# Optimization experiments

Measured on AMD Instinct MI355X. Metric: run time of the kernel, lower is better.

The kernel has to match this reference:

```python
import jax, jax.numpy as jnp
import numpy as np

D_MODEL = 1024
NUM_HEADS = 16
HEAD_DIM = D_MODEL // NUM_HEADS
FF_DIM = 4096
EPS = 1e-5


def _layer_norm(x, gamma, beta):
    mu = jnp.mean(x, axis=-1, keepdims=True)
    var = jnp.var(x, axis=-1, keepdims=True)
    return (x - mu) * jax.lax.rsqrt(var + EPS) * gamma + beta


def setup_inputs() -> dict:
    key0 = jax.random.key(0)
    ks = jax.random.split(key0, 20)
    s = 0.02
    B, S = 2, 2048
    inp = {
        'value': jax.random.normal(ks[0], (B, S, D_MODEL), jnp.float32),
        'key': jax.random.normal(ks[1], (B, S, D_MODEL), jnp.float32),
        'query': jax.random.normal(ks[2], (B, S, D_MODEL), jnp.float32),
        # attention projections (stored [in, out]; y = x @ W + b)
        'wq': jax.random.normal(ks[3], (D_MODEL, D_MODEL), jnp.float32) * s,
        'bq': jnp.zeros((D_MODEL,), jnp.float32),
        'wk': jax.random.normal(ks[4], (D_MODEL, D_MODEL), jnp.float32) * s,
        'bk': jnp.zeros((D_MODEL,), jnp.float32),
        'wv': jax.random.normal(ks[5], (D_MODEL, D_MODEL), jnp.float32) * s,
        'bv': jnp.zeros((D_MODEL,), jnp.float32),
        'wo': jax.random.normal(ks[6], (D_MODEL, D_MODEL), jnp.float32) * s,
        'bo': jnp.zeros((D_MODEL,), jnp.float32),
        # layernorm 1
        'g1': jnp.ones((D_MODEL,), jnp.float32),
        'beta1': jnp.zeros((D_MODEL,), jnp.float32),
        # feed-forward
        'w1': jax.random.normal(ks[7], (D_MODEL, FF_DIM), jnp.float32) * s,
        'b1': jnp.zeros((FF_DIM,), jnp.float32),
        'w2': jax.random.normal(ks[8], (FF_DIM, D_MODEL), jnp.float32) * s,
        'b2': jnp.zeros((D_MODEL,), jnp.float32),
        # layernorm 2
        'g2': jnp.ones((D_MODEL,), jnp.float32),
        'beta2': jnp.zeros((D_MODEL,), jnp.float32),
    }
    return inp


def reference(value, key, query, wq, bq, wk, bk, wv, bv, wo, bo,
              g1, beta1, w1, b1, w2, b2, g2, beta2):
    B, S, _ = query.shape
    # QKV projections -> [B, S, H, Dh]
    Q = (query @ wq + bq).reshape(B, S, NUM_HEADS, HEAD_DIM)
    K = (key @ wk + bk).reshape(B, S, NUM_HEADS, HEAD_DIM)
    V = (value @ wv + bv).reshape(B, S, NUM_HEADS, HEAD_DIM)
    # scaled dot-product attention (full score matrix, as in source)
    energy = jnp.einsum('bqhd,bkhd->bhqk', Q, K) / jnp.sqrt(jnp.float32(HEAD_DIM))
    attn = jax.nn.softmax(energy, axis=-1)
    out = jnp.einsum('bhqk,bkhd->bqhd', attn, V).reshape(B, S, D_MODEL)
    attn_out = out @ wo + bo
    # residual + norm1 (dropout is identity in eval)
    x = _layer_norm(attn_out + query, g1, beta1)
    # feed-forward
    ff = jax.nn.relu(x @ w1 + b1) @ w2 + b2
    # residual + norm2
    return _layer_norm(ff + x, g2, beta2)
```

## Files before the change

### kernel.cpp

```cpp
#include <hip/hip_runtime.h>
#include <hip/hip_bf16.h>
#include <cstdint>
#include <math.h>

typedef __bf16 bf16_t;
typedef __attribute__((ext_vector_type(2))) __bf16 bf16x2;
typedef __attribute__((ext_vector_type(4))) __bf16 bf16x4;
typedef __attribute__((ext_vector_type(8))) __bf16 bf16x8;
typedef __attribute__((ext_vector_type(4))) float f32x4;
typedef __attribute__((ext_vector_type(16))) float f32x16;
typedef __attribute__((ext_vector_type(2))) int int2v;
typedef __attribute__((ext_vector_type(4))) int int4v;

#define B_SZ 2
#define S_SZ 2048
#define D_MODEL 1024
#define NUM_HEADS 16
#define HEAD_DIM 64
#define FF_DIM 4096
#define M_ROWS (B_SZ * S_SZ)

#define CF 0.180336880f
#define THRC 2.0f

__device__ __forceinline__ float fexp2(float x) { return __builtin_amdgcn_exp2f(x); }

__device__ __forceinline__ void gload_lds16(const void* g, void* lds) {
    __builtin_amdgcn_global_load_lds(
        (const __attribute__((address_space(1))) void*)(uintptr_t)g,
        (__attribute__((address_space(3))) void*)(uint32_t)(uintptr_t)lds,
        16, 0, 0);
}

__device__ __forceinline__ f32x4 mfma16(bf16x8 a, bf16x8 b, f32x4 c) {
    return __builtin_amdgcn_mfma_f32_16x16x32_bf16(a, b, c, 0, 0, 0);
}
__device__ __forceinline__ f32x16 mfma32(bf16x8 a, bf16x8 b, f32x16 c) {
    return __builtin_amdgcn_mfma_f32_32x32x16_bf16(a, b, c, 0, 0, 0);
}
__device__ __forceinline__ int2v plswap(int a, int b) {
    return __builtin_amdgcn_permlane32_swap(a, b, false, false);
}
__device__ __forceinline__ int packbf(float a, float b) {
    bf16x2 t; t[0] = (bf16_t)a; t[1] = (bf16_t)b;
    return __builtin_bit_cast(int, t);
}

__device__ __forceinline__ int xcd_swz(int lin, int nwg) {
    return (lin & 7) * (nwg >> 3) + (lin >> 3);
}

__global__ __launch_bounds__(256) void cast3_f32_bf16(const float* __restrict__ in0,
                                                      const float* __restrict__ in1,
                                                      const float* __restrict__ in2,
                                                      bf16_t* __restrict__ out0,
                                                      bf16_t* __restrict__ out1,
                                                      bf16_t* __restrict__ out2) {
    int which = blockIdx.x >> 12;
    int blk = blockIdx.x & 4095;
    const float* in = which == 0 ? in0 : which == 1 ? in1 : in2;
    bf16_t* out = which == 0 ? out0 : which == 1 ? out1 : out2;
    size_t i = ((size_t)blk * 256 + threadIdx.x) * 4;
    float4 v = *(const float4*)(in + i);
    bf16x4 o;
    o[0] = (bf16_t)v.x; o[1] = (bf16_t)v.y; o[2] = (bf16_t)v.z; o[3] = (bf16_t)v.w;
    *(bf16x4*)(out + i) = o;
}

__global__ __launch_bounds__(256) void transpose_cast_w4(const float* __restrict__ W0,
                                                         const float* __restrict__ W1,
                                                         const float* __restrict__ W2,
                                                         const float* __restrict__ W3,
                                                         bf16_t* __restrict__ T0,
                                                         bf16_t* __restrict__ T1,
                                                         bf16_t* __restrict__ T2,
                                                         bf16_t* __restrict__ T3) {
    __shared__ float t[32][33];
    const int K = 1024, N = 1024;
    const float* W = blockIdx.z == 0 ? W0 : blockIdx.z == 1 ? W1 : blockIdx.z == 2 ? W2 : W3;
    bf16_t* WT = blockIdx.z == 0 ? T0 : blockIdx.z == 1 ? T1 : blockIdx.z == 2 ? T2 : T3;
    int tid = threadIdx.x;
    int rr = tid >> 3, cc = (tid & 7) * 4;
    int k0 = blockIdx.x * 32, n0 = blockIdx.y * 32;
    float4 v = *(const float4*)(W + (size_t)(k0 + rr) * N + n0 + cc);
    t[rr][cc + 0] = v.x; t[rr][cc + 1] = v.y; t[rr][cc + 2] = v.z; t[rr][cc + 3] = v.w;
    __syncthreads();
    bf16x4 o;
    o[0] = (bf16_t)t[cc + 0][rr]; o[1] = (bf16_t)t[cc + 1][rr];
    o[2] = (bf16_t)t[cc + 2][rr]; o[3] = (bf16_t)t[cc + 3][rr];
    *(bf16x4*)(WT + (size_t)(n0 + rr) * K + k0 + cc) = o;
}

__global__ __launch_bounds__(256) void transpose_cast_w(const float* __restrict__ W,
                                                        bf16_t* __restrict__ WT,
                                                        int K, int N) {
    __shared__ float t[32][33];
    int tid = threadIdx.x;
    int rr = tid >> 3, cc = (tid & 7) * 4;
    int k0 = blockIdx.x * 32, n0 = blockIdx.y * 32;
    float4 v = *(const float4*)(W + (size_t)(k0 + rr) * N + n0 + cc);
    t[rr][cc + 0] = v.x; t[rr][cc + 1] = v.y; t[rr][cc + 2] = v.z; t[rr][cc + 3] = v.w;
    __syncthreads();
    bf16x4 o;
    o[0] = (bf16_t)t[cc + 0][rr]; o[1] = (bf16_t)t[cc + 1][rr];
    o[2] = (bf16_t)t[cc + 2][rr]; o[3] = (bf16_t)t[cc + 3][rr];
    *(bf16x4*)(WT + (size_t)(n0 + rr) * K + k0 + cc) = o;
}

__global__ __launch_bounds__(256) void transpose_v(const bf16_t* __restrict__ Vp,
                                                   bf16_t* __restrict__ VT) {
    __shared__ bf16_t t[32][34];
    int tid = threadIdx.x;
    int rr = tid >> 3, cc = (tid & 7) * 4;
    int bh = blockIdx.z;
    int b = bh >> 4, h = bh & 15;
    int s0 = blockIdx.x * 32, d0 = blockIdx.y * 32;
    bf16x4 v = *(const bf16x4*)(Vp + ((size_t)(b * S_SZ + s0 + rr)) * D_MODEL + h * HEAD_DIM + d0 + cc);
    t[rr][cc + 0] = v[0]; t[rr][cc + 1] = v[1]; t[rr][cc + 2] = v[2]; t[rr][cc + 3] = v[3];
    __syncthreads();
    bf16x4 o;
    o[0] = t[cc + 0][rr]; o[1] = t[cc + 1][rr]; o[2] = t[cc + 2][rr]; o[3] = t[cc + 3][rr];
    *(bf16x4*)(VT + ((size_t)(bh * HEAD_DIM + d0 + rr)) * S_SZ + s0 + cc) = o;
}

template<int NJT, bool RELU, bool OUT_BF16, bool OUT_F32>
__device__ __forceinline__ void gemm8p_core(const bf16_t* __restrict__ Ag, int lda,
                                            const bf16_t* __restrict__ Bg, int ldb,
                                            const float* __restrict__ bias, bool useBias,
                                            float* __restrict__ Cf,
                                            bf16_t* __restrict__ Cb,
                                            int N, int Klen, int m0, int n0,
                                            bf16_t* sA, bf16_t* sB) {
    constexpr int BELE = 8192 * NJT;
    constexpr int NBQ = 2 * NJT;
    const int tid = threadIdx.x;
    const int lane = tid & 63, w = tid >> 6;
    const int l31 = lane & 31, hi = lane >> 5;
    const int wm = (w >> 2) * 128;
    const int wn = (w & 3) * (32 * NJT);
    const int rs7 = l31 & 7;

    const int scol = ((tid & 7) ^ ((tid >> 3) & 7)) * 8;
    const bf16_t* aSrc = Ag + (size_t)(m0 + (tid >> 3)) * lda + scol;
    const bf16_t* bSrc = Bg + (size_t)(n0 + (tid >> 3)) * ldb + scol;

    f32x16 acc[4][NJT];
#pragma unroll
    for (int it = 0; it < 4; it++)
#pragma unroll
        for (int jt = 0; jt < NJT; jt++)
#pragma unroll
            for (int e = 0; e < 16; e++) acc[it][jt][e] = 0.f;

    auto stA = [&](int buf, int q, int k0) {
        gload_lds16(aSrc + (size_t)(q * 64) * lda + k0, sA + buf * 16384 + q * 4096 + tid * 8);
    };
    auto stB = [&](int buf, int q, int k0) {
        gload_lds16(bSrc + (size_t)(q * 64) * ldb + k0, sB + buf * BELE + q * 4096 + tid * 8);
    };

    bf16x8 a[4], b[NJT];
    auto RD = [&](int buf, int ks) {
        const bf16_t* bA = sA + buf * 16384;
        const bf16_t* bB = sB + buf * BELE;
        const int cs = ((((ks << 1) | hi)) ^ rs7) << 3;
#pragma unroll
        for (int it = 0; it < 4; it++)
            a[it] = *(const bf16x8*)(bA + (wm + it * 32 + l31) * 64 + cs);
#pragma unroll
        for (int jt = 0; jt < NJT; jt++)
            b[jt] = *(const bf16x8*)(bB + (wn + jt * 32 + l31) * 64 + cs);
    };
    auto MM = [&]() {
        __builtin_amdgcn_s_setprio(1);
#pragma unroll
        for (int it = 0; it < 4; it++)
#pragma unroll
            for (int jt = 0; jt < NJT; jt++)
                acc[it][jt] = mfma32(a[it], b[jt], acc[it][jt]);
        __builtin_amdgcn_s_setprio(0);
    };

#define LGKM0() do { asm volatile("s_waitcnt lgkmcnt(0)" ::: "memory"); \
                     __builtin_amdgcn_sched_barrier(0); } while (0)

    const int nk = Klen >> 6;
#pragma unroll
    for (int q = 0; q < 4; q++) stA(0, q, 0);
#pragma unroll
    for (int q = 0; q < NBQ; q++) stB(0, q, 0);
    asm volatile("s_waitcnt vmcnt(0)" ::: "memory");
    __builtin_amdgcn_s_barrier();

    for (int t = 0; t < nk; ++t) {
        const int buf = t & 1, nb = buf ^ 1;
        const int kn = (t + 1) << 6;
        const bool hn = (t + 1 < nk);
        RD(buf, 0);
        if (hn) { stA(nb, 0, kn); stA(nb, 1, kn); stA(nb, 2, kn); }
        LGKM0();
        MM();
        RD(buf, 1);
        if (hn) { stA(nb, 3, kn); stB(nb, 0, kn); if (NBQ > 1) stB(nb, 1, kn); }
        LGKM0();
        MM();
        RD(buf, 2);
        if (hn && NBQ > 2) { stB(nb, 2, kn); stB(nb, 3, kn); }
        LGKM0();
        MM();
        RD(buf, 3);
        LGKM0();
        MM();
        asm volatile("s_waitcnt vmcnt(0)" ::: "memory");
        __builtin_amdgcn_s_barrier();
    }
#undef LGKM0

#pragma unroll
    for (int it = 0; it < 4; it++) {
#pragma unroll
        for (int jt = 0; jt < NJT; jt++) {
            const int n = n0 + wn + jt * 32 + l31;
            const float bv = useBias ? bias[n] : 0.f;
#pragma unroll
            for (int e = 0; e < 16; e++) {
                const int mrow = m0 + wm + it * 32 + (e & 3) + ((e >> 2) << 3) + hi * 4;
                float val = acc[it][jt][e] + bv;
                if (RELU) val = fmaxf(val, 0.f);
                if (OUT_F32) Cf[(size_t)mrow * N + n] = val;
                if (OUT_BF16) Cb[(size_t)mrow * N + n] = (bf16_t)val;
            }
        }
    }
}

template<int NJT, bool RELU>
__global__ __launch_bounds__(512, 1) void gemm8p(const bf16_t* __restrict__ A, int lda,
                                                 const bf16_t* __restrict__ Bt, int ldb,
                                                 const float* __restrict__ bias,
                                                 bf16_t* __restrict__ Cb0,
                                                 bf16_t* __restrict__ Cb1,
                                                 int N, int Klen) {
    __shared__ bf16_t sA[2 * 16384];
    __shared__ bf16_t sB[2 * 8192 * NJT];
    const int lin = blockIdx.x + gridDim.x * (blockIdx.y + gridDim.y * blockIdx.z);
    const int nwg = gridDim.x * gridDim.y * gridDim.z;
    const int sz = xcd_swz(lin, nwg);
    const int bx = sz % gridDim.x;
    const int rest = sz / gridDim.x;
    const int by = rest % gridDim.y;
    const int bz = rest / gridDim.y;
    const int koff = bz * Klen;
    gemm8p_core<NJT, RELU, true, false>(A + koff, lda, Bt + koff, ldb,
                                        bias, bz == 0,
                                        nullptr, bz ? Cb1 : Cb0, N, Klen,
                                        bx * 256, by * (128 * NJT), sA, sB);
}

template<int NJT, bool RELU>
__global__ __launch_bounds__(512, 1) void gemm8p_b(const bf16_t* __restrict__ A, int lda,
                                                   const bf16_t* __restrict__ Bt, int ldb,
                                                   const float* __restrict__ bias,
                                                   bf16_t* __restrict__ Cb,
                                                   int N, int Klen) {
    __shared__ bf16_t sA[2 * 16384];
    __shared__ bf16_t sB[2 * 8192 * NJT];
    const int lin = blockIdx.x + gridDim.x * (blockIdx.y + gridDim.y * blockIdx.z);
    const int nwg = gridDim.x * gridDim.y * gridDim.z;
    const int sz = xcd_swz(lin, nwg);
    const int bx = sz % gridDim.x;
    const int rest = sz / gridDim.x;
    const int by = rest % gridDim.y;
    gemm8p_core<NJT, RELU, true, false>(A, lda, Bt, ldb, bias, true,
                                        nullptr, Cb, N, Klen,
                                        bx * 256, by * (128 * NJT), sA, sB);
}

__global__ __launch_bounds__(512, 1) void gemm_qkv8p(const bf16_t* __restrict__ A0,
                                                     const bf16_t* __restrict__ A1,
                                                     const bf16_t* __restrict__ A2,
                                                     const bf16_t* __restrict__ B0,
                                                     const bf16_t* __restrict__ B1,
                                                     const bf16_t* __restrict__ B2,
                                                     const float* __restrict__ b0,
                                                     const float* __restrict__ b1,
                                                     const float* __restrict__ b2,
                                                     bf16_t* __restrict__ C0,
                                                     bf16_t* __restrict__ C1,
                                                     bf16_t* __restrict__ C2) {
    __shared__ bf16_t sA[2 * 16384];
    __shared__ bf16_t sB[2 * 16384];
    const int lin = blockIdx.x + gridDim.x * (blockIdx.y + gridDim.y * blockIdx.z);
    const int nwg = gridDim.x * gridDim.y * gridDim.z;
    const int sz = xcd_swz(lin, nwg);
    const int bx = sz % gridDim.x;
    const int rest = sz / gridDim.x;
    const int by = rest % gridDim.y;
    const int bz = rest / gridDim.y;
    const bf16_t* A = bz == 0 ? A0 : bz == 1 ? A1 : A2;
    const bf16_t* Bt = bz == 0 ? B0 : bz == 1 ? B1 : B2;
    const float* bias = bz == 0 ? b0 : bz == 1 ? b1 : b2;
    bf16_t* C = bz == 0 ? C0 : bz == 1 ? C1 : C2;
    gemm8p_core<2, false, true, false>(A, 1024, Bt, 1024, bias, true,
                                       nullptr, C, 1024, 1024, bx * 256, by * 256, sA, sB);
}

__device__ __forceinline__ void flash_tile(
    const char* kt, const char* vt, int l31, int hi,
    const bf16x8 (&bq)[4],
    f32x16& o0, f32x16& o1, float& mC, float& l_run)
{
    bf16x8 ak[4];
#pragma unroll
    for (int kb = 0; kb < 4; kb++)
        ak[kb] = *(const bf16x8*)(kt + l31 * 128 + (((kb << 1) | hi) ^ (l31 & 7)) * 16);
    bf16x8 av[4];
#pragma unroll
    for (int db = 0; db < 2; db++)
#pragma unroll
        for (int kb = 0; kb < 2; kb++)
            av[db * 2 + kb] = *(const bf16x8*)(vt + (db * 32 + l31) * 64 + ((((kb << 1) | hi)) ^ ((l31 >> 1) & 3)) * 16);

    f32x16 s;
#pragma unroll
    for (int e = 0; e < 16; e++) s[e] = 0.f;
#pragma unroll
    for (int kb = 0; kb < 4; kb++) s = mfma32(ak[kb], bq[kb], s);

    float ma = fmaxf(fmaxf(s[0], s[1]), fmaxf(s[2], s[3]));
    float mb = fmaxf(fmaxf(s[4], s[5]), fmaxf(s[6], s[7]));
    float mc = fmaxf(fmaxf(s[8], s[9]), fmaxf(s[10], s[11]));
    float md = fmaxf(fmaxf(s[12], s[13]), fmaxf(s[14], s[15]));
    float pmaxC = fmaxf(fmaxf(ma, mb), fmaxf(mc, md)) * CF;

    if (!__all(pmaxC <= mC + THRC)) {
        int2v pr = plswap(__float_as_int(pmaxC), __float_as_int(pmaxC));
        float rowmaxC = fmaxf(__int_as_float(pr[0]), __int_as_float(pr[1]));
        float mnewC = fmaxf(mC, rowmaxC);
        float alpha = fexp2(mC - mnewC);
        mC = mnewC;
        l_run *= alpha;
#pragma unroll
        for (int e = 0; e < 16; e++) { o0[e] *= alpha; o1[e] *= alpha; }
    }

#pragma unroll
    for (int e = 0; e < 16; e++) s[e] = fexp2(__builtin_fmaf(s[e], CF, -mC));
    float t0 = (s[0] + s[1]) + (s[2] + s[3]);
    float t1 = (s[4] + s[5]) + (s[6] + s[7]);
    float t2 = (s[8] + s[9]) + (s[10] + s[11]);
    float t3 = (s[12] + s[13]) + (s[14] + s[15]);
    l_run += (t0 + t1) + (t2 + t3);

#pragma unroll
    for (int kb2 = 0; kb2 < 2; kb2++) {
        const int bse = kb2 * 8;
        int W0 = packbf(s[bse + 0], s[bse + 1]);
        int W1 = packbf(s[bse + 2], s[bse + 3]);
        int W2 = packbf(s[bse + 4], s[bse + 5]);
        int W3 = packbf(s[bse + 6], s[bse + 7]);
        int2v r02 = plswap(W0, W2);
        int2v r13 = plswap(W1, W3);
        int4v fw; fw[0] = r02[0]; fw[1] = r13[0]; fw[2] = r02[1]; fw[3] = r13[1];
        bf16x8 pf = __builtin_bit_cast(bf16x8, fw);
        o0 = mfma32(av[kb2], pf, o0);
        o1 = mfma32(av[2 + kb2], pf, o1);
    }
}

__global__ __launch_bounds__(256) void flash_attn(const bf16_t* __restrict__ Qp,
                                                  const bf16_t* __restrict__ Kp,
                                                  const bf16_t* __restrict__ VT,
                                                  bf16_t* __restrict__ Oa) {
    __shared__ alignas(16) char lds[2][2][8192];
    const int tid = threadIdx.x;
    const int lane = tid & 63;
    const int wave = tid >> 6;
    const int half = wave >> 1;
    const int qt = wave & 1;
    const int l31 = lane & 31, hi = lane >> 5;

    const int lin = blockIdx.x + (blockIdx.y << 5) + (blockIdx.z << 9);
    const int swz = (lin & 7) * 128 + (lin >> 3);
    const int qb = swz & 31;
    const int h = (swz >> 5) & 15;
    const int b = swz >> 9;

    const int q0 = qb * 64 + qt * 32;

    const bf16_t* Qb = Qp + (size_t)b * S_SZ * D_MODEL + h * HEAD_DIM;
    const bf16_t* Kb = Kp + (size_t)b * S_SZ * D_MODEL + h * HEAD_DIM;
    const bf16_t* Vb = VT + ((size_t)(b * NUM_HEADS + h) * HEAD_DIM) * S_SZ;

    const int sh = wave & 1;
    const int skvbase = sh * (S_SZ / 2);
    const bool kRole = wave < 2;

    const bf16_t* src_run;
    size_t inner_stride;
    size_t tile_stride;
    char* dst0;
    char* dst1;
    if (kRole) {
        src_run = Kb + (size_t)(skvbase + (lane >> 3)) * D_MODEL + ((lane & 7) ^ (lane >> 3)) * 8;
        inner_stride = (size_t)8 * D_MODEL;
        tile_stride = (size_t)32 * D_MODEL;
        dst0 = &lds[0][sh][0] + lane * 16;
        dst1 = &lds[1][sh][0] + lane * 16;
    } else {
        src_run = Vb + (size_t)(lane >> 2) * S_SZ + skvbase + ((lane & 3) ^ ((lane >> 3) & 3)) * 8;
        inner_stride = (size_t)16 * S_SZ;
        tile_stride = 32;
        dst0 = &lds[0][sh][4096] + lane * 16;
        dst1 = &lds[1][sh][4096] + lane * 16;
    }

    bf16x8 bq[4];
#pragma unroll
    for (int kb = 0; kb < 4; kb++)
        bq[kb] = *(const bf16x8*)(Qb + (size_t)(q0 + l31) * D_MODEL + kb * 16 + hi * 8);

    f32x16 o0, o1;
#pragma unroll
    for (int e = 0; e < 16; e++) { o0[e] = 0.f; o1[e] = 0.f; }
    float mC = -1e30f, l_run = 0.f;

    const char* kt0 = &lds[0][half][0];
    const char* vt0 = &lds[0][half][4096];
    const char* kt1 = &lds[1][half][0];
    const char* vt1 = &lds[1][half][4096];

#pragma unroll
    for (int ii = 0; ii < 4; ii++)
        gload_lds16(src_run + ii * inner_stride, dst0 + ii * 1024);
    src_run += tile_stride;
    __syncthreads();

    for (int t = 0; t < 32; t += 2) {
#pragma unroll
        for (int ii = 0; ii < 4; ii++)
            gload_lds16(src_run + ii * inner_stride, dst1 + ii * 1024);
        src_run += tile_stride;
        flash_tile(kt0, vt0, l31, hi, bq, o0, o1, mC, l_run);
        __syncthreads();

        if (t + 2 < 32) {
#pragma unroll
            for (int ii = 0; ii < 4; ii++)
                gload_lds16(src_run + ii * inner_stride, dst0 + ii * 1024);
            src_run += tile_stride;
        }
        flash_tile(kt1, vt1, l31, hi, bq, o0, o1, mC, l_run);
        __syncthreads();
    }

    int2v lp = plswap(__float_as_int(l_run), __float_as_int(l_run));
    l_run = __int_as_float(lp[0]) + __int_as_float(lp[1]);

    float (*obuf)[2][64] = (float (*)[2][64])(&lds[0][0][0]);
    float (*mrg)[64][2] = (float (*)[64][2])(&lds[0][0][0] + 16384);
    if (half == 1) {
        mrg[qt][lane][0] = mC;
        mrg[qt][lane][1] = l_run;
#pragma unroll
        for (int e = 0; e < 16; e++) {
            obuf[e][qt][lane] = o0[e];
            obuf[16 + e][qt][lane] = o1[e];
        }
    }
    __syncthreads();
    if (half == 0) {
        const float m2C = mrg[qt][lane][0], l2 = mrg[qt][lane][1];
        const float mm = fmaxf(mC, m2C);
        const float e1 = fexp2(mC - mm);
        const float e2 = fexp2(m2C - mm);
        const float linv = 1.f / (l_run * e1 + l2 * e2);
        bf16_t* Orow = Oa + ((size_t)b * S_SZ + q0 + l31) * D_MODEL + h * HEAD_DIM;
#pragma unroll
        for (int db = 0; db < 2; db++) {
#pragma unroll
            for (int rq = 0; rq < 4; rq++) {
                bf16x4 st;
#pragma unroll
                for (int i = 0; i < 4; i++) {
                    const int e = rq * 4 + i;
                    const float own = db ? o1[e] : o0[e];
                    const float oth = obuf[db * 16 + e][qt][lane];
                    st[i] = (bf16_t)((own * e1 + oth * e2) * linv);
                }
                *(bf16x4*)(Orow + db * 32 + rq * 8 + hi * 4) = st;
            }
        }
    }
}

__global__ __launch_bounds__(256) void ln_fused(const bf16_t* __restrict__ A,
                                                const bf16_t* __restrict__ A2,
                                                const float* __restrict__ R,
                                                const float* __restrict__ gamma,
                                                const float* __restrict__ beta,
                                                float* __restrict__ Xf,
                                                bf16_t* __restrict__ Xb) {
    __shared__ float red[8];
    int row = blockIdx.x, tid = threadIdx.x;
    size_t base = (size_t)row * D_MODEL + tid * 4;
    bf16x4 a = *(const bf16x4*)(A + base);
    bf16x4 a2 = *(const bf16x4*)(A2 + base);
    float4 rv = *(const float4*)(R + base);
    float v0 = (float)a[0] + (float)a2[0] + rv.x;
    float v1 = (float)a[1] + (float)a2[1] + rv.y;
    float v2 = (float)a[2] + (float)a2[2] + rv.z;
    float v3 = (float)a[3] + (float)a2[3] + rv.w;
    float s = v0 + v1 + v2 + v3;
    float q = v0 * v0 + v1 * v1 + v2 * v2 + v3 * v3;
#pragma unroll
    for (int off = 32; off; off >>= 1) { s += __shfl_down(s, off); q += __shfl_down(q, off); }
    if ((tid & 63) == 0) { red[tid >> 6] = s; red[4 + (tid >> 6)] = q; }
    __syncthreads();
    s = red[0] + red[1] + red[2] + red[3];
    q = red[4] + red[5] + red[6] + red[7];
    float mean = s * (1.f / D_MODEL);
    float var = q * (1.f / D_MODEL) - mean * mean;
    float rstd = rsqrtf(var + 1e-5f);
    float4 gm = *(const float4*)(gamma + tid * 4);
    float4 bt = *(const float4*)(beta + tid * 4);
    float y0 = (v0 - mean) * rstd * gm.x + bt.x;
    float y1 = (v1 - mean) * rstd * gm.y + bt.y;
    float y2 = (v2 - mean) * rstd * gm.z + bt.z;
    float y3 = (v3 - mean) * rstd * gm.w + bt.w;
    float4 yo; yo.x = y0; yo.y = y1; yo.z = y2; yo.w = y3;
    *(float4*)(Xf + base) = yo;
    if (Xb) {
        bf16x4 ob; ob[0] = (bf16_t)y0; ob[1] = (bf16_t)y1; ob[2] = (bf16_t)y2; ob[3] = (bf16_t)y3;
        *(bf16x4*)(Xb + base) = ob;
    }
}

extern "C" void kernel_launch(void* const* d_in, const int* in_sizes, int n_in,
                              void* d_out, int out_size, void* d_ws, size_t ws_size,
                              hipStream_t stream) {
    const float* value = (const float*)d_in[0];
    const float* key   = (const float*)d_in[1];
    const float* query = (const float*)d_in[2];
    const float* wq = (const float*)d_in[3];
    const float* bq = (const float*)d_in[4];
    const float* wk = (const float*)d_in[5];
    const float* bk = (const float*)d_in[6];
    const float* wv = (const float*)d_in[7];
    const float* bv = (const float*)d_in[8];
    const float* wo = (const float*)d_in[9];
    const float* bo = (const float*)d_in[10];
    const float* g1 = (const float*)d_in[11];
    const float* beta1 = (const float*)d_in[12];
    const float* w1 = (const float*)d_in[13];
    const float* b1 = (const float*)d_in[14];
    const float* w2 = (const float*)d_in[15];
    const float* b2 = (const float*)d_in[16];
    const float* g2 = (const float*)d_in[17];
    const float* beta2 = (const float*)d_in[18];
    (void)in_sizes; (void)n_in; (void)out_size; (void)ws_size;

    const size_t MB = 1ull << 20;
    char* ws = (char*)d_ws;
    bf16_t* wqT = (bf16_t*)(ws + 0 * MB);
    bf16_t* wkT = (bf16_t*)(ws + 2 * MB);
    bf16_t* wvT = (bf16_t*)(ws + 4 * MB);
    bf16_t* woT = (bf16_t*)(ws + 6 * MB);
    bf16_t* w1T = (bf16_t*)(ws + 8 * MB);
    bf16_t* w2T = (bf16_t*)(ws + 16 * MB);
    bf16_t* q_bf = (bf16_t*)(ws + 24 * MB);
    bf16_t* k_bf = (bf16_t*)(ws + 32 * MB);
    bf16_t* v_bf = (bf16_t*)(ws + 40 * MB);
    bf16_t* Qp  = (bf16_t*)(ws + 48 * MB);
    bf16_t* Kp  = (bf16_t*)(ws + 56 * MB);
    bf16_t* Vp  = (bf16_t*)(ws + 64 * MB);
    bf16_t* VT  = (bf16_t*)(ws + 72 * MB);
    bf16_t* attn = (bf16_t*)(ws + 24 * MB);
    bf16_t* woP0 = (bf16_t*)(ws + 32 * MB);
    bf16_t* woP1 = (bf16_t*)(ws + 42 * MB);
    float*  x_f = (float*)(ws + 80 * MB);
    bf16_t* x_b = (bf16_t*)(ws + 24 * MB);
    bf16_t* h_b = (bf16_t*)(ws + 32 * MB);
    bf16_t* ffP0 = (bf16_t*)(ws + 64 * MB);
    bf16_t* ffP1 = (bf16_t*)(ws + 72 * MB);

    dim3 blk(256);
    dim3 blk512(512);

    cast3_f32_bf16<<<12288, blk, 0, stream>>>(query, key, value, q_bf, k_bf, v_bf);
    transpose_cast_w4<<<dim3(32, 32, 4), blk, 0, stream>>>(wq, wk, wv, wo, wqT, wkT, wvT, woT);
    transpose_cast_w<<<dim3(32, 128), blk, 0, stream>>>(w1, w1T, 1024, 4096);
    transpose_cast_w<<<dim3(128, 32), blk, 0, stream>>>(w2, w2T, 4096, 1024);

    gemm_qkv8p<<<dim3(16, 4, 3), blk512, 0, stream>>>(q_bf, k_bf, v_bf, wqT, wkT, wvT,
                                                      bq, bk, bv, Qp, Kp, Vp);

    transpose_v<<<dim3(64, 2, 32), blk, 0, stream>>>(Vp, VT);

    flash_attn<<<dim3(32, 16, 2), blk, 0, stream>>>(Qp, Kp, VT, attn);

    gemm8p<1, false><<<dim3(16, 8, 2), blk512, 0, stream>>>(attn, 1024, woT, 1024, bo, woP0, woP1, D_MODEL, 512);

    ln_fused<<<4096, blk, 0, stream>>>(woP0, woP1, query, g1, beta1, x_f, x_b);

    gemm8p_b<2, true><<<dim3(16, 16, 1), blk512, 0, stream>>>(x_b, 1024, w1T, 1024, b1, h_b, FF_DIM, 1024);

    gemm8p<1, false><<<dim3(16, 8, 2), blk512, 0, stream>>>(h_b, 4096, w2T, 4096, b2, ffP0, ffP1, D_MODEL, 2048);

    ln_fused<<<4096, blk, 0, stream>>>(ffP0, ffP1, x_f, g2, beta2, (float*)d_out, nullptr);
}
```

Before: 231.9 us.

## Merge input prep kernels and fuse V transpose into QKV GEMM epilogue

Merges the activation cast and all weight transpose-casts into one prep kernel, replacing four launches with one. The V projection GEMM epilogue now writes V already transposed per head into the VT layout, which removes the separate transpose_v kernel and its round trip of V through memory. The tradeoff is that the epilogue's transposed stores are 8-byte scattered writes with a stride of S, so they coalesce less well than the row-major path.

```diff
diff --git a/kernel.cpp b/kernel.cpp
--- a/kernel.cpp
+++ b/kernel.cpp
@@ -50,77 +50,53 @@
     return (lin & 7) * (nwg >> 3) + (lin >> 3);
 }
 
-__global__ __launch_bounds__(256) void cast3_f32_bf16(const float* __restrict__ in0,
-                                                      const float* __restrict__ in1,
-                                                      const float* __restrict__ in2,
-                                                      bf16_t* __restrict__ out0,
-                                                      bf16_t* __restrict__ out1,
-                                                      bf16_t* __restrict__ out2) {
-    int which = blockIdx.x >> 12;
-    int blk = blockIdx.x & 4095;
-    const float* in = which == 0 ? in0 : which == 1 ? in1 : in2;
-    bf16_t* out = which == 0 ? out0 : which == 1 ? out1 : out2;
-    size_t i = ((size_t)blk * 256 + threadIdx.x) * 4;
-    float4 v = *(const float4*)(in + i);
-    bf16x4 o;
-    o[0] = (bf16_t)v.x; o[1] = (bf16_t)v.y; o[2] = (bf16_t)v.z; o[3] = (bf16_t)v.w;
-    *(bf16x4*)(out + i) = o;
-}
-
-__global__ __launch_bounds__(256) void transpose_cast_w4(const float* __restrict__ W0,
-                                                         const float* __restrict__ W1,
-                                                         const float* __restrict__ W2,
-                                                         const float* __restrict__ W3,
-                                                         bf16_t* __restrict__ T0,
-                                                         bf16_t* __restrict__ T1,
-                                                         bf16_t* __restrict__ T2,
-                                                         bf16_t* __restrict__ T3) {
+__global__ __launch_bounds__(256) void prep_all(
+    const float* __restrict__ q, const float* __restrict__ k, const float* __restrict__ v,
+    bf16_t* __restrict__ qb, bf16_t* __restrict__ kb, bf16_t* __restrict__ vb,
+    const float* __restrict__ wq, const float* __restrict__ wk,
+    const float* __restrict__ wv, const float* __restrict__ wo,
+    const float* __restrict__ w1, const float* __restrict__ w2,
+    bf16_t* __restrict__ wqT, bf16_t* __restrict__ wkT,
+    bf16_t* __restrict__ wvT, bf16_t* __restrict__ woT,
+    bf16_t* __restrict__ w1T, bf16_t* __restrict__ w2T) {
     __shared__ float t[32][33];
-    const int K = 1024, N = 1024;
-    const float* W = blockIdx.z == 0 ? W0 : blockIdx.z == 1 ? W1 : blockIdx.z == 2 ? W2 : W3;
-    bf16_t* WT = blockIdx.z == 0 ? T0 : blockIdx.z == 1 ? T1 : blockIdx.z == 2 ? T2 : T3;
-    int tid = threadIdx.x;
-    int rr = tid >> 3, cc = (tid & 7) * 4;
-    int k0 = blockIdx.x * 32, n0 = blockIdx.y * 32;
-    float4 v = *(const float4*)(W + (size_t)(k0 + rr) * N + n0 + cc);
-    t[rr][cc + 0] = v.x; t[rr][cc + 1] = v.y; t[rr][cc + 2] = v.z; t[rr][cc + 3] = v.w;
+    const int id = blockIdx.x;
+    const int tid = threadIdx.x;
+    if (id >= 12288) {
+        const int t2 = id - 12288;
+        const int which = t2 >> 12, blk = t2 & 4095;
+        const float* in = which == 0 ? q : which == 1 ? k : v;
+        bf16_t* out = which == 0 ? qb : which == 1 ? kb : vb;
+        size_t i = ((size_t)blk * 256 + tid) * 4;
+        float4 vv = *(const float4*)(in + i);
+        bf16x4 o;
+        o[0] = (bf16_t)vv.x; o[1] = (bf16_t)vv.y; o[2] = (bf16_t)vv.z; o[3] = (bf16_t)vv.w;
+        *(bf16x4*)(out + i) = o;
+        return;
+    }
+    const float* W; bf16_t* WT; int K, N, k0, n0;
+    if (id < 4096) {
+        const int z = id >> 10, t3 = id & 1023;
+        W = z == 0 ? wq : z == 1 ? wk : z == 2 ? wv : wo;
+        WT = z == 0 ? wqT : z == 1 ? wkT : z == 2 ? wvT : woT;
+        K = 1024; N = 1024; k0 = (t3 & 31) * 32; n0 = (t3 >> 5) * 32;
+    } else if (id < 8192) {
+        const int t3 = id - 4096;
+        W = w1; WT = w1T; K = 1024; N = 4096;
+        k0 = (t3 & 31) * 32; n0 = (t3 >> 5) * 32;
+    } else {
+        const int t3 = id - 8192;
+        W = w2; WT = w2T; K = 4096; N = 1024;
+        k0 = (t3 & 127) * 32; n0 = (t3 >> 7) * 32;
+    }
+    const int rr = tid >> 3, cc = (tid & 7) * 4;
+    float4 vv = *(const float4*)(W + (size_t)(k0 + rr) * N + n0 + cc);
+    t[rr][cc + 0] = vv.x; t[rr][cc + 1] = vv.y; t[rr][cc + 2] = vv.z; t[rr][cc + 3] = vv.w;
     __syncthreads();
     bf16x4 o;
     o[0] = (bf16_t)t[cc + 0][rr]; o[1] = (bf16_t)t[cc + 1][rr];
     o[2] = (bf16_t)t[cc + 2][rr]; o[3] = (bf16_t)t[cc + 3][rr];
     *(bf16x4*)(WT + (size_t)(n0 + rr) * K + k0 + cc) = o;
-}
-
-__global__ __launch_bounds__(256) void transpose_cast_w(const float* __restrict__ W,
-                                                        bf16_t* __restrict__ WT,
-                                                        int K, int N) {
-    __shared__ float t[32][33];
-    int tid = threadIdx.x;
-    int rr = tid >> 3, cc = (tid & 7) * 4;
-    int k0 = blockIdx.x * 32, n0 = blockIdx.y * 32;
-    float4 v = *(const float4*)(W + (size_t)(k0 + rr) * N + n0 + cc);
-    t[rr][cc + 0] = v.x; t[rr][cc + 1] = v.y; t[rr][cc + 2] = v.z; t[rr][cc + 3] = v.w;
-    __syncthreads();
-    bf16x4 o;
-    o[0] = (bf16_t)t[cc + 0][rr]; o[1] = (bf16_t)t[cc + 1][rr];
-    o[2] = (bf16_t)t[cc + 2][rr]; o[3] = (bf16_t)t[cc + 3][rr];
-    *(bf16x4*)(WT + (size_t)(n0 + rr) * K + k0 + cc) = o;
-}
-
-__global__ __launch_bounds__(256) void transpose_v(const bf16_t* __restrict__ Vp,
-                                                   bf16_t* __restrict__ VT) {
-    __shared__ bf16_t t[32][34];
-    int tid = threadIdx.x;
-    int rr = tid >> 3, cc = (tid & 7) * 4;
-    int bh = blockIdx.z;
-    int b = bh >> 4, h = bh & 15;
-    int s0 = blockIdx.x * 32, d0 = blockIdx.y * 32;
-    bf16x4 v = *(const bf16x4*)(Vp + ((size_t)(b * S_SZ + s0 + rr)) * D_MODEL + h * HEAD_DIM + d0 + cc);
-    t[rr][cc + 0] = v[0]; t[rr][cc + 1] = v[1]; t[rr][cc + 2] = v[2]; t[rr][cc + 3] = v[3];
-    __syncthreads();
-    bf16x4 o;
-    o[0] = t[cc + 0][rr]; o[1] = t[cc + 1][rr]; o[2] = t[cc + 2][rr]; o[3] = t[cc + 3][rr];
-    *(bf16x4*)(VT + ((size_t)(bh * HEAD_DIM + d0 + rr)) * S_SZ + s0 + cc) = o;
 }
 
 template<int NJT, bool RELU, bool OUT_BF16, bool OUT_F32>
@@ -130,7 +106,8 @@
                                             float* __restrict__ Cf,
                                             bf16_t* __restrict__ Cb,
                                             int N, int Klen, int m0, int n0,
-                                            bf16_t* sA, bf16_t* sB) {
+                                            bf16_t* sA, bf16_t* sB,
+                                            bf16_t* __restrict__ VTt) {
     constexpr int BELE = 8192 * NJT;
     constexpr int NBQ = 2 * NJT;
     const int tid = threadIdx.x;
@@ -216,6 +193,28 @@
     }
 #undef LGKM0
 
+    if (VTt) {
+#pragma unroll
+        for (int it = 0; it < 4; it++) {
+#pragma unroll
+            for (int jt = 0; jt < NJT; jt++) {
+                const int n = n0 + wn + jt * 32 + l31;
+                const float bv = bias[n];
+                const int hh = n >> 6, dd = n & 63;
+#pragma unroll
+                for (int rq = 0; rq < 4; rq++) {
+                    bf16x4 st;
+#pragma unroll
+                    for (int i2 = 0; i2 < 4; i2++)
+                        st[i2] = (bf16_t)(acc[it][jt][rq * 4 + i2] + bv);
+                    const int mrow = m0 + wm + it * 32 + rq * 8 + hi * 4;
+                    const int bb = mrow >> 11, s = mrow & 2047;
+                    *(bf16x4*)(VTt + (((size_t)(bb * 16 + hh)) * 64 + dd) * 2048 + s) = st;
+                }
+            }
+        }
+        return;
+    }
 #pragma unroll
     for (int it = 0; it < 4; it++) {
 #pragma unroll
@@ -254,7 +253,7 @@
     gemm8p_core<NJT, RELU, true, false>(A + koff, lda, Bt + koff, ldb,
                                         bias, bz == 0,
                                         nullptr, bz ? Cb1 : Cb0, N, Klen,
-                                        bx * 256, by * (128 * NJT), sA, sB);
+                                        bx * 256, by * (128 * NJT), sA, sB, nullptr);
 }
 
 template<int NJT, bool RELU>
@@ -273,7 +272,7 @@
     const int by = rest % gridDim.y;
     gemm8p_core<NJT, RELU, true, false>(A, lda, Bt, ldb, bias, true,
                                         nullptr, Cb, N, Klen,
-                                        bx * 256, by * (128 * NJT), sA, sB);
+                                        bx * 256, by * (128 * NJT), sA, sB, nullptr);
 }
 
 __global__ __launch_bounds__(512, 1) void gemm_qkv8p(const bf16_t* __restrict__ A0,
@@ -287,7 +286,7 @@
                                                      const float* __restrict__ b2,
                                                      bf16_t* __restrict__ C0,
                                                      bf16_t* __restrict__ C1,
-                                                     bf16_t* __restrict__ C2) {
+                                                     bf16_t* __restrict__ VTout) {
     __shared__ bf16_t sA[2 * 16384];
     __shared__ bf16_t sB[2 * 16384];
     const int lin = blockIdx.x + gridDim.x * (blockIdx.y + gridDim.y * blockIdx.z);
@@ -300,9 +299,11 @@
     const bf16_t* A = bz == 0 ? A0 : bz == 1 ? A1 : A2;
     const bf16_t* Bt = bz == 0 ? B0 : bz == 1 ? B1 : B2;
     const float* bias = bz == 0 ? b0 : bz == 1 ? b1 : b2;
-    bf16_t* C = bz == 0 ? C0 : bz == 1 ? C1 : C2;
+    bf16_t* C = bz == 0 ? C0 : bz == 1 ? C1 : nullptr;
+    bf16_t* VTt = bz == 2 ? VTout : nullptr;
     gemm8p_core<2, false, true, false>(A, 1024, Bt, 1024, bias, true,
-                                       nullptr, C, 1024, 1024, bx * 256, by * 256, sA, sB);
+                                       nullptr, C, 1024, 1024, bx * 256, by * 256,
+                                       sA, sB, VTt);
 }
 
 __device__ __forceinline__ void flash_tile(
@@ -573,8 +574,7 @@
     bf16_t* v_bf = (bf16_t*)(ws + 40 * MB);
     bf16_t* Qp  = (bf16_t*)(ws + 48 * MB);
     bf16_t* Kp  = (bf16_t*)(ws + 56 * MB);
-    bf16_t* Vp  = (bf16_t*)(ws + 64 * MB);
-    bf16_t* VT  = (bf16_t*)(ws + 72 * MB);
+    bf16_t* VT  = (bf16_t*)(ws + 64 * MB);
     bf16_t* attn = (bf16_t*)(ws + 24 * MB);
     bf16_t* woP0 = (bf16_t*)(ws + 32 * MB);
     bf16_t* woP1 = (bf16_t*)(ws + 42 * MB);
@@ -587,15 +587,12 @@
     dim3 blk(256);
     dim3 blk512(512);
 
-    cast3_f32_bf16<<<12288, blk, 0, stream>>>(query, key, value, q_bf, k_bf, v_bf);
-    transpose_cast_w4<<<dim3(32, 32, 4), blk, 0, stream>>>(wq, wk, wv, wo, wqT, wkT, wvT, woT);
-    transpose_cast_w<<<dim3(32, 128), blk, 0, stream>>>(w1, w1T, 1024, 4096);
-    transpose_cast_w<<<dim3(128, 32), blk, 0, stream>>>(w2, w2T, 4096, 1024);
+    prep_all<<<24576, blk, 0, stream>>>(query, key, value, q_bf, k_bf, v_bf,
+                                        wq, wk, wv, wo, w1, w2,
+                                        wqT, wkT, wvT, woT, w1T, w2T);
 
     gemm_qkv8p<<<dim3(16, 4, 3), blk512, 0, stream>>>(q_bf, k_bf, v_bf, wqT, wkT, wvT,
-                                                      bq, bk, bv, Qp, Kp, Vp);
-
-    transpose_v<<<dim3(64, 2, 32), blk, 0, stream>>>(Vp, VT);
+                                                      bq, bk, bv, Qp, Kp, VT);
 
     flash_attn<<<dim3(32, 16, 2), blk, 0, stream>>>(Qp, Kp, VT, attn);
 
```

Result: no change. 227.7 us (median of 2 runs) (-1.8%).
